# Performance work log

Measured on AMD Instinct MI355X. Metric: run time of the kernel, lower is better.

## Reference

```python
import jax, jax.numpy as jnp
from jax import lax
import numpy as np


def _conv(x, w, b, stride=1, pad=1):
    y = lax.conv_general_dilated(x, w, (stride, stride), ((pad, pad), (pad, pad)),
                                 dimension_numbers=('NCHW', 'OIHW', 'NCHW'))
    return y + b[None, :, None, None]


def _deconv(x, w, b):
    # PyTorch ConvTranspose2d(k=3, s=2, p=1, output_padding=1); w is torch layout (Cin, Cout, 3, 3)
    wt = jnp.flip(w, (2, 3)).transpose(1, 0, 2, 3)  # (Cout, Cin, 3, 3)
    y = lax.conv_general_dilated(x, wt, (1, 1), ((1, 2), (1, 2)), lhs_dilation=(2, 2),
                                 dimension_numbers=('NCHW', 'OIHW', 'NCHW'))
    return y + b[None, :, None, None]


def _lrelu(x):
    return jnp.where(x >= 0, x, 0.01 * x)


def _nonlocal(x, tw, tb, pw, pb, gw, gb, ww, wb):
    # embedded-Gaussian non-local block with residual (NONLocalBlock2D)
    B, C, H, W = x.shape
    N = H * W
    th = _conv(x, tw, tb, 1, 0).reshape(B, -1, N)
    ph = _conv(x, pw, pb, 1, 0).reshape(B, -1, N)
    g = _conv(x, gw, gb, 1, 0).reshape(B, -1, N)
    attn = jax.nn.softmax(jnp.einsum('bcn,bcm->bnm', th, ph), axis=-1)  # [B,N,N]
    y = jnp.einsum('bnm,bcm->bcn', attn, g).reshape(B, -1, H, W)
    return _conv(y, ww, wb, 1, 0) + x


def _deform_conv(x, offset, mask, w, b):
    # modulated deformable conv (DCNv2-style), k=3 s=1 p=1, zero padding outside bounds
    B, C, H, W = x.shape
    K2 = 9
    ky, kx = jnp.meshgrid(jnp.arange(3) - 1, jnp.arange(3) - 1, indexing='ij')
    ky = ky.reshape(-1).astype(x.dtype)
    kx = kx.reshape(-1).astype(x.dtype)
    off = offset.reshape(B, K2, 2, H, W)  # (dy, dx) interleaved per kernel tap
    py = jnp.arange(H, dtype=x.dtype)[None, None, :, None] + ky[None, :, None, None] + off[:, :, 0]
    px = jnp.arange(W, dtype=x.dtype)[None, None, None, :] + kx[None, :, None, None] + off[:, :, 1]
    y0 = jnp.floor(py)
    x0 = jnp.floor(px)
    wy1 = py - y0
    wx1 = px - x0
    xf = x.reshape(B, C, H * W)

    def gather(yi, xi):
        valid = ((yi >= 0) & (yi < H) & (xi >= 0) & (xi < W)).astype(x.dtype)
        yc = jnp.clip(yi, 0, H - 1).astype(jnp.int32)
        xc = jnp.clip(xi, 0, W - 1).astype(jnp.int32)
        idx = (yc * W + xc).reshape(B, 1, K2 * H * W)
        v = jnp.take_along_axis(xf, idx, axis=2).reshape(B, C, K2, H, W)
        return v * valid[:, None]

    val = (gather(y0, x0) * ((1 - wy1) * (1 - wx1))[:, None]
           + gather(y0, x0 + 1) * ((1 - wy1) * wx1)[:, None]
           + gather(y0 + 1, x0) * (wy1 * (1 - wx1))[:, None]
           + gather(y0 + 1, x0 + 1) * (wy1 * wx1)[:, None])
    val = val * mask[:, None]  # modulation
    return jnp.einsum('bckhw,ock->bohw', val, w.reshape(w.shape[0], C, K2)) + b[None, :, None, None]


def _forward(x_all, ms_fine, ms_coarse, enc_w0, enc_b0, enc_w1, enc_b1,
             nl0_tw, nl0_tb, nl0_pw, nl0_pb, nl0_gw, nl0_gb, nl0_ww, nl0_wb,
             nl1_tw, nl1_tb, nl1_pw, nl1_pb, nl1_gw, nl1_gb, nl1_ww, nl1_wb,
             dec_w0, dec_b0, dec_w1, dec_b1, off_w, off_b, dcn_w, dcn_b):
    def motion(pc, cc, pf, cf):
        # scale 0 (coarse, reversed order), mot_mode='concat'
        e0 = _lrelu(_conv(jnp.concatenate([pc, cc], 1), enc_w0, enc_b0, 2, 1))
        m0 = e0 + _nonlocal(e0, nl0_tw, nl0_tb, nl0_pw, nl0_pb, nl0_gw, nl0_gb, nl0_ww, nl0_wb)
        u0 = _lrelu(_deconv(m0, dec_w0, dec_b0))
        # scale 1 (fine)
        e1 = _lrelu(_conv(jnp.concatenate([pf, cf], 1), enc_w1, enc_b1, 2, 1))
        m1 = e1 + _nonlocal(e1, nl1_tw, nl1_tb, nl1_pw, nl1_pb, nl1_gw, nl1_gb, nl1_ww, nl1_wb)
        return _lrelu(_deconv(m1 + u0, dec_w1, dec_b1))

    aligned = [x_all[0]]
    for s in range(1, x_all.shape[0]):  # seq_len - 1 alignments
        mot = motion(ms_coarse[s], ms_coarse[0], ms_fine[s], ms_fine[0])
        est = _conv(mot, off_w, off_b, 1, 1)  # [B, 27, H, W]
        offset = est[:, 9:]
        mask = jax.nn.sigmoid(est[:, :9])
        aligned.append(_deform_conv(x_all[s], offset, mask, dcn_w, dcn_b))
    return jnp.stack(aligned)


def setup_inputs() -> dict:
    key = jax.random.key(0)
    ks = iter(jax.random.split(key, 48))

    def rn(shape, scale=1.0):
        return jax.random.normal(next(ks), shape, dtype=jnp.float32) * scale

    S, B = 3, 2
    inp = {
        'x_all': rn((S, B, 128, 128, 128)),
        'ms_fine': rn((S, B, 128, 128, 128)),
        'ms_coarse': rn((S, B, 256, 64, 64)),
        'enc_w0': rn((64, 512, 3, 3), 0.02), 'enc_b0': rn((64,), 0.02),
        'enc_w1': rn((64, 256, 3, 3), 0.02), 'enc_b1': rn((64,), 0.02),
    }
    for i in range(2):
        inp[f'nl{i}_tw'] = rn((32, 64, 1, 1), 0.05); inp[f'nl{i}_tb'] = rn((32,), 0.02)
        inp[f'nl{i}_pw'] = rn((32, 64, 1, 1), 0.05); inp[f'nl{i}_pb'] = rn((32,), 0.02)
        inp[f'nl{i}_gw'] = rn((32, 64, 1, 1), 0.05); inp[f'nl{i}_gb'] = rn((32,), 0.02)
        inp[f'nl{i}_ww'] = rn((64, 32, 1, 1), 0.05); inp[f'nl{i}_wb'] = rn((64,), 0.02)
    inp['dec_w0'] = rn((64, 64, 3, 3), 0.05); inp['dec_b0'] = rn((64,), 0.02)
    inp['dec_w1'] = rn((64, 64, 3, 3), 0.05); inp['dec_b1'] = rn((64,), 0.02)
    inp['off_w'] = rn((27, 64, 3, 3), 0.02); inp['off_b'] = rn((27,), 0.02)
    inp['dcn_w'] = rn((128, 128, 3, 3), 0.03); inp['dcn_b'] = rn((128,), 0.02)
    return inp


def reference(x_all, ms_fine, ms_coarse, enc_w0, enc_b0, enc_w1, enc_b1,
              nl0_tw, nl0_tb, nl0_pw, nl0_pb, nl0_gw, nl0_gb, nl0_ww, nl0_wb,
              nl1_tw, nl1_tb, nl1_pw, nl1_pb, nl1_gw, nl1_gb, nl1_ww, nl1_wb,
              dec_w0, dec_b0, dec_w1, dec_b1, off_w, off_b, dcn_w, dcn_b):
    return _forward(x_all, ms_fine, ms_coarse, enc_w0, enc_b0, enc_w1, enc_b1,
                    nl0_tw, nl0_tb, nl0_pw, nl0_pb, nl0_gw, nl0_gb, nl0_ww, nl0_wb,
                    nl1_tw, nl1_tb, nl1_pw, nl1_pb, nl1_gw, nl1_gb, nl1_ww, nl1_wb,
                    dec_w0, dec_b0, dec_w1, dec_b1, off_w, off_b, dcn_w, dcn_b)
```

## Files before the change

kernel.cpp:

```cpp
#include <hip/hip_runtime.h>
#include <math.h>

typedef __attribute__((ext_vector_type(8))) short bf16x8;
typedef __attribute__((ext_vector_type(4))) float f32x4;
typedef unsigned short ushort_t;
typedef unsigned int uint_t;

__device__ __forceinline__ float lrelu_f(float x) { return x >= 0.f ? x : 0.01f * x; }

__device__ __forceinline__ ushort_t f2bf(float f) {
    uint_t x = __float_as_uint(f);
    uint_t r = (x + 0x7fffu + ((x >> 16) & 1u)) >> 16;
    return (ushort_t)r;
}

__device__ __forceinline__ uint_t pack_bf16(float lo, float hi) {
    uint_t out;
    asm("v_cvt_pk_bf16_f32 %0, %1, %2" : "=v"(out) : "v"(lo), "v"(hi));
    return out;
}

__device__ __forceinline__ float fexp2(float x) {
    float r;
    asm("v_exp_f32 %0, %1" : "=v"(r) : "v"(x));
    return r;
}

__global__ __launch_bounds__(256) void castw2_kernel(const float* __restrict__ w,
    ushort_t* __restrict__ w2, int Cout, int Cin, int K, int deconv)
{
    int idx = blockIdx.x * 256 + threadIdx.x;
    if (idx >= 64 * K) return;
    int co = idx / K, kp = idx % K;
    int cb = kp / 288;
    int r  = kp % 288;
    int tap = r >> 5, cl = r & 31;
    int ci = cb * 32 + cl;
    float val = 0.f;
    if (co < Cout)
        val = deconv ? w[(size_t)(ci * Cout + co) * 9 + (8 - tap)]
                     : w[(size_t)(co * Cin + ci) * 9 + tap];
    w2[idx] = f2bf(val);
}

template<int STRIDE, int MODE>
__global__ __launch_bounds__(256) void conv3x3_mfma(
    const float* __restrict__ inA, const float* __restrict__ inB, int CinA,
    size_t sStrideA, int Hin, int Win, int Cin,
    const ushort_t* __restrict__ w2, int K,
    int Wout, int Npx, int tilesPerMap, int ksplit, int chunksPerKs,
    float* __restrict__ part,
    const float* __restrict__ bias, int act, int CoutStore, float* __restrict__ outDirect)
{
    __shared__ ushort_t sB[64 * 40];
    int tile = blockIdx.x % tilesPerMap;
    int ks   = (blockIdx.x / tilesPerMap) % ksplit;
    int b4   = blockIdx.x / (tilesPerMap * ksplit);
    int s_idx = b4 >> 1, bb = b4 & 1;
    int tid  = threadIdx.x;
    int wave = tid >> 6, lane = tid & 63;
    int lrow = lane & 15, lkg = lane >> 4;
    int px  = tid & 63;
    int cio = wave * 8;
    int p   = tile * 64 + px;
    int oy  = p / Wout, ox = p - oy * Wout;
    int HWin = Hin * Win;
    int CinB = Cin - CinA;

    f32x4 acc[4];
    #pragma unroll
    for (int n2 = 0; n2 < 4; ++n2) acc[n2] = (f32x4){0.f, 0.f, 0.f, 0.f};

    for (int cch = 0; cch < chunksPerKs; ++cch) {
        int chunkIdx = ks * chunksPerKs + cch;
        int cb  = chunkIdx / 9;
        int tap = chunkIdx - cb * 9;
        int cib = cb * 32;
        int ky = tap / 3, kx = tap - ky * 3;
        float msk;
        int offp;
        if (MODE == 0) {
            int iy = oy * STRIDE - 1 + ky;
            int ix = ox * STRIDE - 1 + kx;
            bool vld = (iy >= 0) && (iy < Hin) && (ix >= 0) && (ix < Win);
            msk = vld ? 1.f : 0.f;
            offp = min(max(iy, 0), Hin - 1) * Win + min(max(ix, 0), Win - 1);
        } else {
            int uy = oy + ky, ux = ox + kx;
            int r = (uy - 1) >> 1, q = (ux - 1) >> 1;
            bool vld = (uy & 1) && (ux & 1) && (r < Hin) && (q < Win);
            msk = vld ? 1.f : 0.f;
            offp = min(max(r, 0), Hin - 1) * Win + min(max(q, 0), Win - 1);
        }
        int c = cib + cio;
        const float* src = (c < CinA)
            ? inA + s_idx * sStrideA + (size_t)(bb * CinA + c) * HWin
            : inB + (size_t)(bb * CinB + (c - CinA)) * HWin;
        float v[8];
        #pragma unroll
        for (int j = 0; j < 8; ++j) v[j] = src[(size_t)j * HWin + offp] * msk;
        uint4 pk;
        pk.x = pack_bf16(v[0], v[1]);
        pk.y = pack_bf16(v[2], v[3]);
        pk.z = pack_bf16(v[4], v[5]);
        pk.w = pack_bf16(v[6], v[7]);
        __syncthreads();
        *(uint4*)&sB[px * 40 + cio] = pk;
        __syncthreads();

        const ushort_t* wr = w2 + (size_t)(wave * 16 + lrow) * K + chunkIdx * 32 + lkg * 8;
        bf16x8 afr = *(const bf16x8*)wr;
        #pragma unroll
        for (int n2 = 0; n2 < 4; ++n2) {
            bf16x8 bfr = *(const bf16x8*)&sB[(n2 * 16 + lrow) * 40 + lkg * 8];
            acc[n2] = __builtin_amdgcn_mfma_f32_16x16x32_bf16(afr, bfr, acc[n2], 0, 0, 0);
        }
    }

    if (bias) {
        #pragma unroll
        for (int n2 = 0; n2 < 4; ++n2) {
            #pragma unroll
            for (int j = 0; j < 4; ++j) {
                int co = wave * 16 + lkg * 4 + j;
                if (co < CoutStore) {
                    int pp = tile * 64 + n2 * 16 + lrow;
                    float r = acc[n2][j] + bias[co];
                    if (act) r = lrelu_f(r);
                    outDirect[((size_t)(b4 * CoutStore + co)) * (size_t)Npx + pp] = r;
                }
            }
        }
    } else {
        #pragma unroll
        for (int n2 = 0; n2 < 4; ++n2) {
            #pragma unroll
            for (int j = 0; j < 4; ++j) {
                int co = wave * 16 + lkg * 4 + j;
                int pp = tile * 64 + n2 * 16 + lrow;
                part[((size_t)(ks * 4 + b4) * 64 + co) * (size_t)Npx + pp] = acc[n2][j];
            }
        }
    }
}

__global__ __launch_bounds__(256) void reduce_bias_act(const float* __restrict__ part,
    const float* __restrict__ bias, float* __restrict__ out,
    int Cout, int Npx, int ksplit, int act)
{
    int idx = blockIdx.x * 256 + threadIdx.x;
    int total = 4 * Cout * Npx;
    if (idx >= total) return;
    int p  = idx % Npx;
    int co = (idx / Npx) % Cout;
    int b4 = idx / (Npx * Cout);
    float s = bias[co];
    for (int ks = 0; ks < ksplit; ++ks)
        s += part[(((size_t)ks * 4 + b4) * 64 + co) * (size_t)Npx + p];
    if (act) s = lrelu_f(s);
    out[((size_t)b4 * Cout + co) * (size_t)Npx + p] = s;
}

__global__ __launch_bounds__(256) void castw_perm_kernel(const float* __restrict__ w,
    ushort_t* __restrict__ wbf)
{
    int idx = blockIdx.x * 256 + threadIdx.x;
    if (idx >= 147456) return;
    int co = idx / 1152;
    int r  = idx % 1152;
    int chunk = r / 288;
    int r2 = r % 288;
    int tap = r2 >> 5;
    int cl  = r2 & 31;
    int ci = chunk * 32 + cl;
    wbf[idx] = f2bf(w[(size_t)co * 1152 + ci * 9 + tap]);
}

__global__ __launch_bounds__(256) void transpose_nhwc_bf16(const float* __restrict__ x,
    ushort_t* __restrict__ xT)
{
    __shared__ float t[32][33];
    int cT = blockIdx.x & 3;
    int pT = (blockIdx.x >> 2) & 511;
    int b4 = blockIdx.x >> 11;
    int tx = threadIdx.x & 31, ty = threadIdx.x >> 5;
    const float* src = x + ((size_t)((b4 + 2) * 128) + cT * 32) * 16384 + (size_t)pT * 32;
    #pragma unroll
    for (int i = 0; i < 4; ++i)
        t[ty + 8 * i][tx] = src[(size_t)(ty + 8 * i) * 16384 + tx];
    __syncthreads();
    ushort_t* dst = xT + ((size_t)b4 * 16384 + (size_t)pT * 32) * 128 + cT * 32;
    #pragma unroll
    for (int i = 0; i < 4; ++i)
        dst[(size_t)(ty + 8 * i) * 128 + tx] = f2bf(t[tx][ty + 8 * i]);
}

__global__ __launch_bounds__(256) void conv1x1x3_bf16(const float* __restrict__ e, int N,
    const float* __restrict__ tw, const float* __restrict__ tb,
    const float* __restrict__ pw, const float* __restrict__ pb,
    const float* __restrict__ gw, const float* __restrict__ gb,
    ushort_t* __restrict__ thT, ushort_t* __restrict__ phT, ushort_t* __restrict__ gT)
{
    __shared__ float sw[32 * 64];
    __shared__ float sb[32];
    int tid = threadIdx.x;
    int idx = blockIdx.x * 256 + tid;
    int j = idx / (4 * N);
    const float* wsel = (j == 0) ? tw : (j == 1) ? pw : gw;
    const float* bsel = (j == 0) ? tb : (j == 1) ? pb : gb;
    for (int i = tid; i < 2048; i += 256) sw[i] = wsel[i];
    if (tid < 32) sb[tid] = bsel[tid];
    __syncthreads();
    int rem = idx - j * 4 * N;
    int n = rem % N, b4 = rem / N;
    float ein[64];
    const float* ep = e + (size_t)b4 * 64 * N + n;
    #pragma unroll
    for (int ci = 0; ci < 64; ++ci) ein[ci] = ep[(size_t)ci * N];

    float val[32];
    #pragma unroll
    for (int cc = 0; cc < 32; ++cc) {
        float acc = sb[cc];
        const float* wr = &sw[cc * 64];
        #pragma unroll
        for (int ci = 0; ci < 64; ++ci) acc = fmaf(wr[ci], ein[ci], acc);
        val[cc] = acc;
    }
    if (j == 0) {
        #pragma unroll
        for (int cc = 0; cc < 32; ++cc) val[cc] *= 1.44269504f;
    }
    if (j < 2) {
        ushort_t* row = (j == 0 ? thT : phT) + ((size_t)b4 * N + n) * 32;
        #pragma unroll
        for (int w4 = 0; w4 < 4; ++w4) {
            uint4 pk;
            pk.x = pack_bf16(val[8 * w4 + 0], val[8 * w4 + 1]);
            pk.y = pack_bf16(val[8 * w4 + 2], val[8 * w4 + 3]);
            pk.z = pack_bf16(val[8 * w4 + 4], val[8 * w4 + 5]);
            pk.w = pack_bf16(val[8 * w4 + 6], val[8 * w4 + 7]);
            *(uint4*)(row + 8 * w4) = pk;
        }
    } else {
        #pragma unroll
        for (int cc = 0; cc < 32; ++cc)
            gT[((size_t)b4 * 32 + cc) * N + n] = f2bf(val[cc]);
    }
}

__global__ __launch_bounds__(256) void attn_flash(const ushort_t* __restrict__ thT,
    const ushort_t* __restrict__ phT, const ushort_t* __restrict__ gT,
    float* __restrict__ partO, float* __restrict__ partML, int N, int KVS)
{
    __shared__ ushort_t sP[4][16 * 40];
    int tid  = threadIdx.x;
    int wave = tid >> 6, lane = tid & 63;
    int lq = lane & 15, lkg = lane >> 4;
    int nqb = N / 64;
    int ks = blockIdx.x % KVS;
    int qb = (blockIdx.x / KVS) % nqb;
    int b4 = blockIdx.x / (KVS * nqb);
    int q0w = qb * 64 + wave * 16;
    int chunk = N / KVS;
    int m_start = ks * chunk;

    bf16x8 qf = *(const bf16x8*)(thT + ((size_t)b4 * N + q0w + lq) * 32 + 8 * lkg);

    float m_run = -1e30f, l_run = 0.f;
    f32x4 acc[2];
    acc[0] = (f32x4){0.f, 0.f, 0.f, 0.f};
    acc[1] = (f32x4){0.f, 0.f, 0.f, 0.f};

    for (int m0 = m_start; m0 < m_start + chunk; m0 += 64) {
        f32x4 tf[4];
        #pragma unroll
        for (int f = 0; f < 4; ++f) {
            bf16x8 kf = *(const bf16x8*)(phT + ((size_t)b4 * N + m0 + f * 16 + lq) * 32 + 8 * lkg);
            tf[f] = __builtin_amdgcn_mfma_f32_16x16x32_bf16(kf, qf,
                        (f32x4){0.f, 0.f, 0.f, 0.f}, 0, 0, 0);
        }

        float mx = -1e30f;
        #pragma unroll
        for (int f = 0; f < 4; ++f)
            #pragma unroll
            for (int r = 0; r < 4; ++r) mx = fmaxf(mx, tf[f][r]);
        mx = fmaxf(mx, __shfl_xor(mx, 16));
        mx = fmaxf(mx, __shfl_xor(mx, 32));

        if (__any(mx > m_run)) {
            float m_new = fmaxf(m_run, mx);
            float scale = fexp2(m_run - m_new);
            l_run *= scale;
            m_run = m_new;
            float sc[4];
            #pragma unroll
            for (int r = 0; r < 4; ++r) sc[r] = __shfl(scale, 4 * lkg + r);
            #pragma unroll
            for (int h = 0; h < 2; ++h)
                #pragma unroll
                for (int r = 0; r < 4; ++r) acc[h][r] *= sc[r];
        }

        float rs = 0.f;
        #pragma unroll
        for (int f = 0; f < 4; ++f)
            #pragma unroll
            for (int r = 0; r < 4; ++r) {
                float pv = fexp2(tf[f][r] - m_run);
                tf[f][r] = pv;
                rs += pv;
            }
        rs += __shfl_xor(rs, 16);
        rs += __shfl_xor(rs, 32);
        l_run += rs;

        #pragma unroll
        for (int f = 0; f < 4; ++f) {
            *(uint_t*)&sP[wave][lq * 40 + f * 16 + 4 * lkg]     = pack_bf16(tf[f][0], tf[f][1]);
            *(uint_t*)&sP[wave][lq * 40 + f * 16 + 4 * lkg + 2] = pack_bf16(tf[f][2], tf[f][3]);
        }

        #pragma unroll
        for (int mc = 0; mc < 2; ++mc) {
            bf16x8 pf = *(const bf16x8*)&sP[wave][lq * 40 + mc * 32 + 8 * lkg];
            #pragma unroll
            for (int h = 0; h < 2; ++h) {
                bf16x8 vf = *(const bf16x8*)(gT + ((size_t)b4 * 32 + h * 16 + lq) * N
                                             + m0 + mc * 32 + 8 * lkg);
                acc[h] = __builtin_amdgcn_mfma_f32_16x16x32_bf16(pf, vf, acc[h], 0, 0, 0);
            }
        }
    }

    #pragma unroll
    for (int h = 0; h < 2; ++h) {
        #pragma unroll
        for (int r = 0; r < 4; ++r) {
            int q = q0w + 4 * lkg + r;
            partO[(((size_t)ks * 4 + b4) * N + q) * 32 + h * 16 + lq] = acc[h][r];
        }
    }
    if (lane < 16) {
        size_t mlo = (((size_t)ks * 4 + b4) * N + q0w + lq) * 2;
        partML[mlo]     = m_run;
        partML[mlo + 1] = l_run;
    }
}

__global__ __launch_bounds__(256) void nl_merge_fused(const float* __restrict__ e,
    const float* __restrict__ partO, const float* __restrict__ partML,
    const float* __restrict__ u,
    const float* __restrict__ ww, const float* __restrict__ wb,
    float* __restrict__ out, int N, int KVS)
{
    __shared__ float sw[64 * 32];
    __shared__ float sb[64];
    int tid = threadIdx.x;
    for (int i = tid; i < 2048; i += 256) sw[i] = ww[i];
    if (tid < 64) sb[tid] = wb[tid];
    __syncthreads();
    int idx = blockIdx.x * 256 + tid;
    int n = idx % N;
    int cog = (idx / N) & 3;
    int b4 = idx / (4 * N);

    float mstar = -1e30f;
    for (int ks = 0; ks < KVS; ++ks)
        mstar = fmaxf(mstar, partML[(((size_t)ks * 4 + b4) * N + n) * 2]);
    float denom = 0.f;
    float yv[32];
    #pragma unroll
    for (int c = 0; c < 32; ++c) yv[c] = 0.f;
    for (int ks = 0; ks < KVS; ++ks) {
        size_t mlo = (((size_t)ks * 4 + b4) * N + n) * 2;
        float w = fexp2(partML[mlo] - mstar);
        denom += w * partML[mlo + 1];
        const f32x4* op = (const f32x4*)(partO + (((size_t)ks * 4 + b4) * N + n) * 32);
        #pragma unroll
        for (int jj = 0; jj < 8; ++jj) {
            f32x4 v = op[jj];
            #pragma unroll
            for (int t = 0; t < 4; ++t) yv[4 * jj + t] = fmaf(w, v[t], yv[4 * jj + t]);
        }
    }
    float inv = 1.f / denom;
    #pragma unroll
    for (int i = 0; i < 16; ++i) {
        int co = cog * 16 + i;
        float dot = 0.f;
        const float* wr = &sw[co * 32];
        #pragma unroll
        for (int c = 0; c < 32; ++c) dot = fmaf(wr[c], yv[c], dot);
        size_t o = (size_t)b4 * 64 * N + (size_t)co * N + n;
        float r = sb[co] + inv * dot + 2.f * e[o];
        if (u) r += u[o];
        out[o] = r;
    }
}

__global__ __launch_bounds__(256) void deform_mfma4(const ushort_t* __restrict__ xT,
    const float* __restrict__ est, const ushort_t* __restrict__ wbf,
    const float* __restrict__ bias, float* __restrict__ out)
{
    const int H = 128, W = 128, HW = 16384;
    const int BS = 296;
    __shared__ ushort_t sB[64 * BS];
    __shared__ float4 sW[576];
    __shared__ uint2  sO[576];
    int id  = blockIdx.x;
    int lin = (id & 7) * 128 + (id >> 3);
    int tile = lin & 255;
    int b4   = lin >> 8;
    int p0   = tile * 64;
    int tid  = threadIdx.x;

    const float* eb = est + (size_t)b4 * 27 * HW;
    for (int i = tid; i < 576; i += 256) {
        int k = i >> 6, j = i & 63;
        int p = p0 + j;
        int yy = p >> 7, xx = p & 127;
        float oy = eb[(size_t)(9 + 2 * k) * HW + p];
        float ox = eb[(size_t)(10 + 2 * k) * HW + p];
        float mv = eb[(size_t)k * HW + p];
        float mk = 1.f / (1.f + __expf(-mv));
        float py = (float)(yy + (k / 3) - 1) + oy;
        float qx = (float)(xx + (k % 3) - 1) + ox;
        float fy0 = floorf(py), fx0 = floorf(qx);
        float wy = py - fy0, wx = qx - fx0;
        int y0 = (int)fy0, x0 = (int)fx0;
        int y1 = y0 + 1, x1 = x0 + 1;
        bool yv0 = (y0 >= 0) && (y0 < H), yv1 = (y1 >= 0) && (y1 < H);
        bool xv0 = (x0 >= 0) && (x0 < W), xv1 = (x1 >= 0) && (x1 < W);
        int y0c = min(max(y0, 0), H - 1), y1c = min(max(y1, 0), H - 1);
        int x0c = min(max(x0, 0), W - 1), x1c = min(max(x1, 0), W - 1);
        float4 w4;
        w4.x = (yv0 && xv0) ? (1.f - wy) * (1.f - wx) * mk : 0.f;
        w4.y = (yv0 && xv1) ? (1.f - wy) * wx * mk : 0.f;
        w4.z = (yv1 && xv0) ? wy * (1.f - wx) * mk : 0.f;
        w4.w = (yv1 && xv1) ? wy * wx * mk : 0.f;
        sW[i] = w4;
        uint_t o00 = (uint_t)(y0c * W + x0c), o01 = (uint_t)(y0c * W + x1c);
        uint_t o10 = (uint_t)(y1c * W + x0c), o11 = (uint_t)(y1c * W + x1c);
        sO[i] = (uint2){ o00 | (o01 << 16), o10 | (o11 << 16) };
    }

    int wave = tid >> 6, lane = tid & 63;
    int co_base = wave * 32;
    int lrow = lane & 15, lkg = lane >> 4;

    f32x4 acc[2][4];
    #pragma unroll
    for (int m2 = 0; m2 < 2; ++m2)
        #pragma unroll
        for (int n2 = 0; n2 < 4; ++n2) acc[m2][n2] = (f32x4){0.f, 0.f, 0.f, 0.f};

    const ushort_t* xb = xT + (size_t)b4 * HW * 128;

    for (int cc = 0; cc < 128; cc += 32) {
        __syncthreads();
        #pragma unroll 3
        for (int it = 0; it < 9; ++it) {
            int task = it * 256 + tid;
            int cg = task & 3;
            int si = task >> 2;
            float4 w4 = sW[si];
            uint2 o4 = sO[si];
            int chb = cc + cg * 8;
            uint4 u00 = *(const uint4*)(xb + (size_t)(o4.x & 0xFFFFu) * 128 + chb);
            uint4 u01 = *(const uint4*)(xb + (size_t)(o4.x >> 16) * 128 + chb);
            uint4 u10 = *(const uint4*)(xb + (size_t)(o4.y & 0xFFFFu) * 128 + chb);
            uint4 u11 = *(const uint4*)(xb + (size_t)(o4.y >> 16) * 128 + chb);
            float v[8];
            const uint_t* a0 = (const uint_t*)&u00;
            const uint_t* a1 = (const uint_t*)&u01;
            const uint_t* a2 = (const uint_t*)&u10;
            const uint_t* a3 = (const uint_t*)&u11;
            #pragma unroll
            for (int q = 0; q < 4; ++q) {
                float c00l = __uint_as_float(a0[q] << 16), c00h = __uint_as_float(a0[q] & 0xffff0000u);
                float c01l = __uint_as_float(a1[q] << 16), c01h = __uint_as_float(a1[q] & 0xffff0000u);
                float c10l = __uint_as_float(a2[q] << 16), c10h = __uint_as_float(a2[q] & 0xffff0000u);
                float c11l = __uint_as_float(a3[q] << 16), c11h = __uint_as_float(a3[q] & 0xffff0000u);
                v[2 * q]     = w4.x * c00l + w4.y * c01l + w4.z * c10l + w4.w * c11l;
                v[2 * q + 1] = w4.x * c00h + w4.y * c01h + w4.z * c10h + w4.w * c11h;
            }
            int pxl = si & 63, tap = si >> 6;
            uint4 pk;
            pk.x = pack_bf16(v[0], v[1]);
            pk.y = pack_bf16(v[2], v[3]);
            pk.z = pack_bf16(v[4], v[5]);
            pk.w = pack_bf16(v[6], v[7]);
            *(uint4*)&sB[pxl * BS + tap * 32 + cg * 8] = pk;
        }
        __syncthreads();
        int kbase = cc * 9;
        #pragma unroll
        for (int ks = 0; ks < 9; ++ks) {
            bf16x8 afr[2], bfr[4];
            #pragma unroll
            for (int m2 = 0; m2 < 2; ++m2)
                afr[m2] = *reinterpret_cast<const bf16x8*>(
                    wbf + (size_t)(co_base + m2 * 16 + lrow) * 1152 + kbase + ks * 32 + lkg * 8);
            #pragma unroll
            for (int n2 = 0; n2 < 4; ++n2)
                bfr[n2] = *reinterpret_cast<const bf16x8*>(
                    &sB[(n2 * 16 + lrow) * BS + ks * 32 + lkg * 8]);
            #pragma unroll
            for (int m2 = 0; m2 < 2; ++m2)
                #pragma unroll
                for (int n2 = 0; n2 < 4; ++n2)
                    acc[m2][n2] = __builtin_amdgcn_mfma_f32_16x16x32_bf16(
                        afr[m2], bfr[n2], acc[m2][n2], 0, 0, 0);
        }
    }

    #pragma unroll
    for (int m2 = 0; m2 < 2; ++m2) {
        #pragma unroll
        for (int j = 0; j < 4; ++j) {
            int co = co_base + m2 * 16 + lkg * 4 + j;
            float bb = bias[co];
            #pragma unroll
            for (int n2 = 0; n2 < 4; ++n2) {
                int px = p0 + n2 * 16 + lrow;
                out[((size_t)((b4 + 2) * 128 + co)) * HW + px] = acc[m2][n2][j] + bb;
            }
        }
    }
}

extern "C" void kernel_launch(void* const* d_in, const int* in_sizes, int n_in,
                              void* d_out, int out_size, void* d_ws, size_t ws_size,
                              hipStream_t stream)
{
    const float* x_all     = (const float*)d_in[0];
    const float* ms_fine   = (const float*)d_in[1];
    const float* ms_coarse = (const float*)d_in[2];
    const float* enc_w0 = (const float*)d_in[3];
    const float* enc_b0 = (const float*)d_in[4];
    const float* enc_w1 = (const float*)d_in[5];
    const float* enc_b1 = (const float*)d_in[6];
    const float* nl_tw[2] = { (const float*)d_in[7],  (const float*)d_in[15] };
    const float* nl_tb[2] = { (const float*)d_in[8],  (const float*)d_in[16] };
    const float* nl_pw[2] = { (const float*)d_in[9],  (const float*)d_in[17] };
    const float* nl_pb[2] = { (const float*)d_in[10], (const float*)d_in[18] };
    const float* nl_gw[2] = { (const float*)d_in[11], (const float*)d_in[19] };
    const float* nl_gb[2] = { (const float*)d_in[12], (const float*)d_in[20] };
    const float* nl_ww[2] = { (const float*)d_in[13], (const float*)d_in[21] };
    const float* nl_wb[2] = { (const float*)d_in[14], (const float*)d_in[22] };
    const float* dec_w0 = (const float*)d_in[23];
    const float* dec_b0 = (const float*)d_in[24];
    const float* dec_w1 = (const float*)d_in[25];
    const float* dec_b1 = (const float*)d_in[26];
    const float* off_w  = (const float*)d_in[27];
    const float* off_b  = (const float*)d_in[28];
    const float* dcn_w  = (const float*)d_in[29];
    const float* dcn_b  = (const float*)d_in[30];

    float* ws = (float*)d_ws;
    ushort_t* wbf     = (ushort_t*)ws;
    ushort_t* w2_enc0 = wbf + 147456;
    ushort_t* w2_enc1 = w2_enc0 + 294912;
    ushort_t* w2_dec0 = w2_enc1 + 147456;
    ushort_t* w2_dec1 = w2_dec0 + 36864;
    ushort_t* w2_est  = w2_dec1 + 36864;
    float* U1      = ws + 350208;
    float* u0      = U1 + 1048576;
    float* e1      = u0 + 1048576;
    float* partML  = e1 + 1048576;
    float* regPart = partML + 262144;
    float* regMot  = regPart + 2097152;

    float* e0 = U1;
    ushort_t* thT0 = (ushort_t*)(U1 + 262144);
    ushort_t* phT0 = thT0 + 131072;
    ushort_t* gT0  = phT0 + 131072;
    float* m0 = U1 + 458752;
    ushort_t* thT1 = (ushort_t*)U1;
    ushort_t* phT1 = thT1 + 524288;
    ushort_t* gT1  = phT1 + 524288;
    float* m1  = U1;
    float* mot = regMot;
    ushort_t* xTb = (ushort_t*)regMot;
    float* est = regPart;
    float* partO1 = regMot;

    float* out = (float*)d_out;
    const size_t frame  = (size_t)2 * 128 * 128 * 128;
    const size_t cframe = (size_t)2 * 256 * 64 * 64;

    hipMemcpyAsync(out, x_all, frame * sizeof(float), hipMemcpyDeviceToDevice, stream);

    castw_perm_kernel<<<(147456 + 255) / 256, 256, 0, stream>>>(dcn_w, wbf);
    castw2_kernel<<<(64 * 4608 + 255) / 256, 256, 0, stream>>>(enc_w0, w2_enc0, 64, 512, 4608, 0);
    castw2_kernel<<<(64 * 2304 + 255) / 256, 256, 0, stream>>>(enc_w1, w2_enc1, 64, 256, 2304, 0);
    castw2_kernel<<<(64 * 576 + 255) / 256, 256, 0, stream>>>(dec_w0, w2_dec0, 64, 64, 576, 1);
    castw2_kernel<<<(64 * 576 + 255) / 256, 256, 0, stream>>>(dec_w1, w2_dec1, 64, 64, 576, 1);
    castw2_kernel<<<(64 * 576 + 255) / 256, 256, 0, stream>>>(off_w, w2_est, 27, 64, 576, 0);


    conv3x3_mfma<2, 0><<<4 * 16 * 8, 256, 0, stream>>>(
        ms_coarse + cframe, ms_coarse, 256, cframe, 64, 64, 512,
        w2_enc0, 4608, 32, 1024, 16, 8, 18, regPart, nullptr, 0, 0, nullptr);
    reduce_bias_act<<<1024, 256, 0, stream>>>(regPart, enc_b0, e0, 64, 1024, 8, 1);

    conv1x1x3_bf16<<<48, 256, 0, stream>>>(e0, 1024,
        nl_tw[0], nl_tb[0], nl_pw[0], nl_pb[0], nl_gw[0], nl_gb[0], thT0, phT0, gT0);
    attn_flash<<<4 * 16 * 8, 256, 0, stream>>>(thT0, phT0, gT0, regPart, partML, 1024, 8);
    nl_merge_fused<<<64, 256, 0, stream>>>(e0, regPart, partML, nullptr,
        nl_ww[0], nl_wb[0], m0, 1024, 8);

    conv3x3_mfma<1, 1><<<4 * 64 * 2, 256, 0, stream>>>(
        m0, m0, 64, (size_t)2 * 64 * 1024, 32, 32, 64,
        w2_dec0, 576, 64, 4096, 64, 2, 9, regPart, nullptr, 0, 0, nullptr);
    reduce_bias_act<<<4096, 256, 0, stream>>>(regPart, dec_b0, u0, 64, 4096, 2, 1);

    conv3x3_mfma<2, 0><<<4 * 64 * 2, 256, 0, stream>>>(
        ms_fine + frame, ms_fine, 128, frame, 128, 128, 256,
        w2_enc1, 2304, 64, 4096, 64, 2, 36, regPart, nullptr, 0, 0, nullptr);
    reduce_bias_act<<<4096, 256, 0, stream>>>(regPart, enc_b1, e1, 64, 4096, 2, 1);

    conv1x1x3_bf16<<<192, 256, 0, stream>>>(e1, 4096,
        nl_tw[1], nl_tb[1], nl_pw[1], nl_pb[1], nl_gw[1], nl_gb[1], thT1, phT1, gT1);
    attn_flash<<<4 * 64 * 8, 256, 0, stream>>>(thT1, phT1, gT1, partO1, partML, 4096, 8);
    nl_merge_fused<<<256, 256, 0, stream>>>(e1, partO1, partML, u0,
        nl_ww[1], nl_wb[1], m1, 4096, 8);

    conv3x3_mfma<1, 1><<<4 * 256, 256, 0, stream>>>(
        m1, m1, 64, (size_t)2 * 64 * 4096, 64, 64, 64,
        w2_dec1, 576, 128, 16384, 256, 1, 18, regPart, dec_b1, 1, 64, mot);

    conv3x3_mfma<1, 0><<<4 * 256, 256, 0, stream>>>(
        mot, mot, 64, (size_t)2 * 64 * 16384, 128, 128, 64,
        w2_est, 576, 128, 16384, 256, 1, 18, regPart, off_b, 0, 27, est);

    transpose_nhwc_bf16<<<8192, 256, 0, stream>>>(x_all, xTb);
    deform_mfma4<<<1024, 256, 0, stream>>>(xTb, est, wbf, dcn_b, out);
}
```

Baseline: 363.6 us.

## Double-buffer conv staging, keep deform sample weights in registers, raise split-K counts

The 3x3 MFMA conv now double-buffers its shared-memory B tile, so the next chunk's gather and pack overlap the current chunk's MFMAs with one barrier per iteration instead of two. The deformable conv kernel precomputes its bilinear weights and offsets into per-thread registers rather than shared memory, and adds an occupancy hint to launch bounds. Several small-resolution convs and the first attention call use larger split-K or KV-split factors for more parallelism, with partials moved to a different scratch region. The costs are more LDS per conv block, higher register pressure in the deform kernel, and extra reduction work.

```diff
diff --git a/kernel.cpp b/kernel.cpp
--- a/kernel.cpp
+++ b/kernel.cpp
@@ -52,7 +52,7 @@
     float* __restrict__ part,
     const float* __restrict__ bias, int act, int CoutStore, float* __restrict__ outDirect)
 {
-    __shared__ ushort_t sB[64 * 40];
+    __shared__ ushort_t sB[2][64 * 40];
     int tile = blockIdx.x % tilesPerMap;
     int ks   = (blockIdx.x / tilesPerMap) % ksplit;
     int b4   = blockIdx.x / (tilesPerMap * ksplit);
@@ -67,12 +67,7 @@
     int HWin = Hin * Win;
     int CinB = Cin - CinA;
 
-    f32x4 acc[4];
-    #pragma unroll
-    for (int n2 = 0; n2 < 4; ++n2) acc[n2] = (f32x4){0.f, 0.f, 0.f, 0.f};
-
-    for (int cch = 0; cch < chunksPerKs; ++cch) {
-        int chunkIdx = ks * chunksPerKs + cch;
+    auto stage_pk = [&](int chunkIdx) -> uint4 {
         int cb  = chunkIdx / 9;
         int tap = chunkIdx - cb * 9;
         int cib = cb * 32;
@@ -104,17 +99,35 @@
         pk.y = pack_bf16(v[2], v[3]);
         pk.z = pack_bf16(v[4], v[5]);
         pk.w = pack_bf16(v[6], v[7]);
+        return pk;
+    };
+
+    f32x4 acc[4];
+    #pragma unroll
+    for (int n2 = 0; n2 < 4; ++n2) acc[n2] = (f32x4){0.f, 0.f, 0.f, 0.f};
+
+    int chunk0 = ks * chunksPerKs;
+    {
+        uint4 pk = stage_pk(chunk0);
+        *(uint4*)&sB[0][px * 40 + cio] = pk;
+    }
+    __syncthreads();
+
+    int cur = 0;
+    for (int cch = 0; cch < chunksPerKs; ++cch) {
+        if (cch + 1 < chunksPerKs) {
+            uint4 pk = stage_pk(chunk0 + cch + 1);
+            *(uint4*)&sB[cur ^ 1][px * 40 + cio] = pk;
+        }
+        const ushort_t* wr = w2 + (size_t)(wave * 16 + lrow) * K + (chunk0 + cch) * 32 + lkg * 8;
+        bf16x8 afr = *(const bf16x8*)wr;
+        #pragma unroll
+        for (int n2 = 0; n2 < 4; ++n2) {
+            bf16x8 bfr = *(const bf16x8*)&sB[cur][(n2 * 16 + lrow) * 40 + lkg * 8];
+            acc[n2] = __builtin_amdgcn_mfma_f32_16x16x32_bf16(afr, bfr, acc[n2], 0, 0, 0);
+        }
         __syncthreads();
-        *(uint4*)&sB[px * 40 + cio] = pk;
-        __syncthreads();
-
-        const ushort_t* wr = w2 + (size_t)(wave * 16 + lrow) * K + chunkIdx * 32 + lkg * 8;
-        bf16x8 afr = *(const bf16x8*)wr;
-        #pragma unroll
-        for (int n2 = 0; n2 < 4; ++n2) {
-            bf16x8 bfr = *(const bf16x8*)&sB[(n2 * 16 + lrow) * 40 + lkg * 8];
-            acc[n2] = __builtin_amdgcn_mfma_f32_16x16x32_bf16(afr, bfr, acc[n2], 0, 0, 0);
-        }
+        cur ^= 1;
     }
 
     if (bias) {
@@ -400,15 +413,13 @@
     }
 }
 
-__global__ __launch_bounds__(256) void deform_mfma4(const ushort_t* __restrict__ xT,
+__global__ __launch_bounds__(256, 4) void deform_mfma5(const ushort_t* __restrict__ xT,
     const float* __restrict__ est, const ushort_t* __restrict__ wbf,
     const float* __restrict__ bias, float* __restrict__ out)
 {
     const int H = 128, W = 128, HW = 16384;
     const int BS = 296;
     __shared__ ushort_t sB[64 * BS];
-    __shared__ float4 sW[576];
-    __shared__ uint2  sO[576];
     int id  = blockIdx.x;
     int lin = (id & 7) * 128 + (id >> 3);
     int tile = lin & 255;
@@ -416,9 +427,13 @@
     int p0   = tile * 64;
     int tid  = threadIdx.x;
 
+    float4 rW[9];
+    uint2  rO[9];
     const float* eb = est + (size_t)b4 * 27 * HW;
-    for (int i = tid; i < 576; i += 256) {
-        int k = i >> 6, j = i & 63;
+    #pragma unroll
+    for (int it = 0; it < 9; ++it) {
+        int si = (it * 256 + tid) >> 2;
+        int k = si >> 6, j = si & 63;
         int p = p0 + j;
         int yy = p >> 7, xx = p & 127;
         float oy = eb[(size_t)(9 + 2 * k) * HW + p];
@@ -440,15 +455,17 @@
         w4.y = (yv0 && xv1) ? (1.f - wy) * wx * mk : 0.f;
         w4.z = (yv1 && xv0) ? wy * (1.f - wx) * mk : 0.f;
         w4.w = (yv1 && xv1) ? wy * wx * mk : 0.f;
-        sW[i] = w4;
+        rW[it] = w4;
         uint_t o00 = (uint_t)(y0c * W + x0c), o01 = (uint_t)(y0c * W + x1c);
         uint_t o10 = (uint_t)(y1c * W + x0c), o11 = (uint_t)(y1c * W + x1c);
-        sO[i] = (uint2){ o00 | (o01 << 16), o10 | (o11 << 16) };
+        rO[it] = (uint2){ o00 | (o01 << 16), o10 | (o11 << 16) };
     }
 
     int wave = tid >> 6, lane = tid & 63;
     int co_base = wave * 32;
     int lrow = lane & 15, lkg = lane >> 4;
+    int cg  = tid & 3;
+    int pxl_base = (tid >> 2);
 
     f32x4 acc[2][4];
     #pragma unroll
@@ -460,13 +477,11 @@
 
     for (int cc = 0; cc < 128; cc += 32) {
         __syncthreads();
-        #pragma unroll 3
+        #pragma unroll
         for (int it = 0; it < 9; ++it) {
-            int task = it * 256 + tid;
-            int cg = task & 3;
-            int si = task >> 2;
-            float4 w4 = sW[si];
-            uint2 o4 = sO[si];
+            int si = (it * 256 + tid) >> 2;
+            float4 w4 = rW[it];
+            uint2 o4 = rO[it];
             int chb = cc + cg * 8;
             uint4 u00 = *(const uint4*)(xb + (size_t)(o4.x & 0xFFFFu) * 128 + chb);
             uint4 u01 = *(const uint4*)(xb + (size_t)(o4.x >> 16) * 128 + chb);
@@ -601,26 +616,26 @@
     castw2_kernel<<<(64 * 576 + 255) / 256, 256, 0, stream>>>(off_w, w2_est, 27, 64, 576, 0);
 
 
-    conv3x3_mfma<2, 0><<<4 * 16 * 8, 256, 0, stream>>>(
+    conv3x3_mfma<2, 0><<<4 * 16 * 16, 256, 0, stream>>>(
         ms_coarse + cframe, ms_coarse, 256, cframe, 64, 64, 512,
-        w2_enc0, 4608, 32, 1024, 16, 8, 18, regPart, nullptr, 0, 0, nullptr);
-    reduce_bias_act<<<1024, 256, 0, stream>>>(regPart, enc_b0, e0, 64, 1024, 8, 1);
+        w2_enc0, 4608, 32, 1024, 16, 16, 9, regMot, nullptr, 0, 0, nullptr);
+    reduce_bias_act<<<1024, 256, 0, stream>>>(regMot, enc_b0, e0, 64, 1024, 16, 1);
 
     conv1x1x3_bf16<<<48, 256, 0, stream>>>(e0, 1024,
         nl_tw[0], nl_tb[0], nl_pw[0], nl_pb[0], nl_gw[0], nl_gb[0], thT0, phT0, gT0);
-    attn_flash<<<4 * 16 * 8, 256, 0, stream>>>(thT0, phT0, gT0, regPart, partML, 1024, 8);
+    attn_flash<<<4 * 16 * 16, 256, 0, stream>>>(thT0, phT0, gT0, regPart, partML, 1024, 16);
     nl_merge_fused<<<64, 256, 0, stream>>>(e0, regPart, partML, nullptr,
-        nl_ww[0], nl_wb[0], m0, 1024, 8);
-
-    conv3x3_mfma<1, 1><<<4 * 64 * 2, 256, 0, stream>>>(
+        nl_ww[0], nl_wb[0], m0, 1024, 16);
+
+    conv3x3_mfma<1, 1><<<4 * 64 * 3, 256, 0, stream>>>(
         m0, m0, 64, (size_t)2 * 64 * 1024, 32, 32, 64,
-        w2_dec0, 576, 64, 4096, 64, 2, 9, regPart, nullptr, 0, 0, nullptr);
-    reduce_bias_act<<<4096, 256, 0, stream>>>(regPart, dec_b0, u0, 64, 4096, 2, 1);
-
-    conv3x3_mfma<2, 0><<<4 * 64 * 2, 256, 0, stream>>>(
+        w2_dec0, 576, 64, 4096, 64, 3, 6, regMot, nullptr, 0, 0, nullptr);
+    reduce_bias_act<<<4096, 256, 0, stream>>>(regMot, dec_b0, u0, 64, 4096, 3, 1);
+
+    conv3x3_mfma<2, 0><<<4 * 64 * 4, 256, 0, stream>>>(
         ms_fine + frame, ms_fine, 128, frame, 128, 128, 256,
-        w2_enc1, 2304, 64, 4096, 64, 2, 36, regPart, nullptr, 0, 0, nullptr);
-    reduce_bias_act<<<4096, 256, 0, stream>>>(regPart, enc_b1, e1, 64, 4096, 2, 1);
+        w2_enc1, 2304, 64, 4096, 64, 4, 18, regMot, nullptr, 0, 0, nullptr);
+    reduce_bias_act<<<4096, 256, 0, stream>>>(regMot, enc_b1, e1, 64, 4096, 4, 1);
 
     conv1x1x3_bf16<<<192, 256, 0, stream>>>(e1, 4096,
         nl_tw[1], nl_tb[1], nl_pw[1], nl_pb[1], nl_gw[1], nl_gb[1], thT1, phT1, gT1);
@@ -637,5 +652,5 @@
         w2_est, 576, 128, 16384, 256, 1, 18, regPart, off_b, 0, 27, est);
 
     transpose_nhwc_bf16<<<8192, 256, 0, stream>>>(x_all, xTb);
-    deform_mfma4<<<1024, 256, 0, stream>>>(xTb, est, wbf, dcn_b, out);
-}
+    deform_mfma5<<<1024, 256, 0, stream>>>(xTb, est, wbf, dcn_b, out);
+}
```

Result: slower. 432.1 us (+18.8%).
